# Optimization experiments

Hardware: AMD Instinct MI355X
Metric: run time of the kernel (lower is better)

## Reference

```python
import jax, jax.numpy as jnp
import numpy as np

B, S, DMODEL = 1, 2048, 4096
H, HKV, DH = 32, 8, 128
LTAB, RBKT = 20, 128
NEG = -1e9


def rotate_half(x):
    x1, x2 = x[..., : x.shape[-1] // 2], x[..., x.shape[-1] // 2:]
    return jnp.concatenate((-x2, x1), axis=-1)


def setup_inputs() -> dict:
    key = jax.random.key(0)
    ks = jax.random.split(key, 12)
    inp = {
        "hidden_states": jax.random.normal(ks[0], (B, S, DMODEL), jnp.float32),
        "cos": jax.random.uniform(ks[1], (B, S, DH), jnp.float32),
        "sin": jax.random.uniform(ks[2], (B, S, DH), jnp.float32),
        "q_probs": jax.random.uniform(ks[3], (B, H, LTAB, RBKT), jnp.float32),
        "v_norm": jax.random.uniform(ks[4], (B, H, S), jnp.float32),
        "allowed": jnp.ones((B, H, S), dtype=bool),
        "k_hard": jax.random.randint(ks[5], (B, H, LTAB, S), 0, RBKT, jnp.int32),
        "Wq": jax.random.normal(ks[6], (DMODEL, H * DH), jnp.float32) * 0.02,
        "Wk": jax.random.normal(ks[7], (DMODEL, HKV * DH), jnp.float32) * 0.02,
        "Wv": jax.random.normal(ks[8], (DMODEL, HKV * DH), jnp.float32) * 0.02,
        "Wo": jax.random.normal(ks[9], (H * DH, DMODEL), jnp.float32) * 0.02,
        "sink": 4,
        "window": 128,
        "M": 256,
    }
    return inp


def _sparse_key_mask(q_probs, v_norm, allowed, k_hard, sink, window, M):
    """Faithful jax version of build_sparse_list_decode, returned as a boolean
    allowed-key mask [B, H, T] (equivalent to scattering sparse_list)."""
    Bm, Hm, _, T = k_hard.shape
    # soft-hash collision score: sum over tables of q bucket prob at key's bucket,
    # weighted by value-norm history, restricted to allowed keys.
    coll = jnp.take_along_axis(q_probs, k_hard.astype(jnp.int32), axis=-1).sum(axis=2)  # [B,H,T]
    scores = jnp.where(allowed, coll * v_norm, -jnp.inf)
    M_eff = min(M, T)
    mask = jnp.zeros((Bm, Hm, T), dtype=bool)
    if M_eff > 0:
        heavy_idx = jax.lax.top_k(scores, M_eff)[1]  # [B,H,M]
        b_ix = jnp.arange(Bm)[:, None, None]
        h_ix = jnp.arange(Hm)[None, :, None]
        mask = mask.at[b_ix, h_ix, heavy_idx].set(True)
    sink = max(0, min(sink, T))
    window = max(0, min(window, T))
    if sink > 0:
        mask = mask.at[:, :, :sink].set(True)
    if window > 0:
        win_start = max(T - window, sink)
        if win_start < T:
            mask = mask.at[:, :, win_start:].set(True)
    if sink == 0 and window == 0:
        mask = mask.at[:, :, T - 1].set(True)
    return mask & allowed


def reference(hidden_states, cos, sin, q_probs, v_norm, allowed, k_hard,
              Wq, Wk, Wv, Wo, sink, window, M):
    Bx, Sx, _ = hidden_states.shape
    scaling = DH ** -0.5
    q = (hidden_states @ Wq).reshape(Bx, Sx, H, DH).transpose(0, 2, 1, 3)   # [B,H,S,Dh]
    k = (hidden_states @ Wk).reshape(Bx, Sx, HKV, DH).transpose(0, 2, 1, 3)  # [B,Hkv,S,Dh]
    v = (hidden_states @ Wv).reshape(Bx, Sx, HKV, DH).transpose(0, 2, 1, 3)
    # RoPE (unsqueeze_dim=1)
    c, s = cos[:, None, :, :], sin[:, None, :, :]
    q = q * c + rotate_half(q) * s
    k = k * c + rotate_half(k) * s
    # repeat_kv for GQA
    n_rep = H // HKV
    k = jnp.repeat(k, n_rep, axis=1)
    v = jnp.repeat(v, n_rep, axis=1)
    # sparse heavy-hitter + sink + window key mask (no_grad in the original)
    key_mask = _sparse_key_mask(q_probs, v_norm, allowed, k_hard, sink, window, M)  # [B,H,S]
    causal = jnp.tril(jnp.ones((Sx, Sx), dtype=bool))
    allow = causal[None, None] & key_mask[:, :, None, :]  # [B,H,S,S]
    scores = jnp.einsum('bhqd,bhkd->bhqk', q, k) * scaling
    attn = jax.nn.softmax(jnp.where(allow, scores, NEG), axis=-1)
    out = jnp.einsum('bhqk,bhkd->bhqd', attn, v)
    out = out.transpose(0, 2, 1, 3).reshape(Bx, Sx, H * DH)
    return out @ Wo
```

## Files before the change

kernel.cpp:

```cpp
#include <hip/hip_runtime.h>
#include <hip/hip_bf16.h>
#include <cstdint>
#include <cstddef>

namespace {

constexpr int S_LEN = 2048;
constexpr int DM    = 4096;
constexpr int NH    = 32;
constexpr int NKV   = 8;
constexpr int DH    = 128;
constexpr int LTAB  = 20;
constexpr int RBKT  = 128;
constexpr int NQKV  = NH * DH + 2 * NKV * DH;
constexpr int KOFF  = NH * DH;
constexpr int VOFF  = NH * DH + NKV * DH;

typedef short s16x8 __attribute__((ext_vector_type(8)));
typedef float f32x4 __attribute__((ext_vector_type(4)));
typedef unsigned long long u64;
struct u64x2 { u64 x, y; };

__device__ inline short bf16s(float f) {
  __hip_bfloat16 b = __float2bfloat16(f);
  return (short)*reinterpret_cast<unsigned short*>(&b);
}
__device__ inline float s2f(short s) {
  unsigned short u = (unsigned short)s;
  return __bfloat162float(*reinterpret_cast<__hip_bfloat16*>(&u));
}

__global__ __launch_bounds__(256) void cvt_f32_bf16(const float* __restrict__ in,
                                                    __hip_bfloat16* __restrict__ out,
                                                    int n4) {
  int i = blockIdx.x * blockDim.x + threadIdx.x;
  if (i >= n4) return;
  float4 v = reinterpret_cast<const float4*>(in)[i];
  ushort4 o;
  o.x = (unsigned short)bf16s(v.x);
  o.y = (unsigned short)bf16s(v.y);
  o.z = (unsigned short)bf16s(v.z);
  o.w = (unsigned short)bf16s(v.w);
  reinterpret_cast<ushort4*>(out)[i] = o;
}

__global__ __launch_bounds__(256) void transpose_cvt64(const float* __restrict__ W,
                                                       __hip_bfloat16* __restrict__ Wt,
                                                       int K, int N) {
  __shared__ float tile[64][65];
  const int kb = blockIdx.y * 64, nb = blockIdx.x * 64;
  const int tid = threadIdx.x;
  const int r0 = tid >> 4, c4 = (tid & 15) * 4;
#pragma unroll
  for (int it = 0; it < 4; ++it) {
    const int r = r0 + it * 16;
    float4 v = *reinterpret_cast<const float4*>(&W[(size_t)(kb + r) * N + nb + c4]);
    tile[r][c4] = v.x;
    tile[r][c4 + 1] = v.y;
    tile[r][c4 + 2] = v.z;
    tile[r][c4 + 3] = v.w;
  }
  __syncthreads();
  const int n0 = tid >> 4, k4 = (tid & 15) * 4;
#pragma unroll
  for (int it = 0; it < 4; ++it) {
    const int n = n0 + it * 16;
    ushort4 o;
    o.x = (unsigned short)bf16s(tile[k4][n]);
    o.y = (unsigned short)bf16s(tile[k4 + 1][n]);
    o.z = (unsigned short)bf16s(tile[k4 + 2][n]);
    o.w = (unsigned short)bf16s(tile[k4 + 3][n]);
    *reinterpret_cast<ushort4*>(&Wt[(size_t)(nb + n) * K + kb + k4]) = o;
  }
}

template <bool OUT_F32>
__global__ __launch_bounds__(256) void gemm_bt(const __hip_bfloat16* __restrict__ A,
                                               const __hip_bfloat16* __restrict__ Bt,
                                               void* __restrict__ Cout,
                                               int N, int K) {
  __shared__ __hip_bfloat16 As[128 * 64];
  __shared__ __hip_bfloat16 Bs[128 * 64];
  const int tid = threadIdx.x;
  const int wid = tid >> 6;
  const int lane = tid & 63;
  const int bm = blockIdx.y, bn = blockIdx.x;
  const int wr = wid >> 1, wc = wid & 1;
  f32x4 acc[4][4] = {};
  const __hip_bfloat16* Abase = A + (size_t)bm * 128 * K;
  const __hip_bfloat16* Bbase = Bt + (size_t)bn * 128 * K;
  for (int kt = 0; kt < K; kt += 64) {
    __syncthreads();
#pragma unroll
    for (int j = 0; j < 4; ++j) {
      const int pb = j * 4096 + wid * 1024;
      const int p = pb + lane * 16;
      const int row = p >> 7;
      const int slot = ((p >> 4) & 7) ^ (row & 7);
      const int goff = row * K + kt + slot * 8;
      __builtin_amdgcn_global_load_lds(
          (const __attribute__((address_space(1))) void*)(Abase + goff),
          (__attribute__((address_space(3))) void*)(As + (pb >> 1)), 16, 0, 0);
      __builtin_amdgcn_global_load_lds(
          (const __attribute__((address_space(1))) void*)(Bbase + goff),
          (__attribute__((address_space(3))) void*)(Bs + (pb >> 1)), 16, 0, 0);
    }
    __syncthreads();
#pragma unroll
    for (int kk = 0; kk < 2; ++kk) {
      s16x8 af[4], bf[4];
#pragma unroll
      for (int i = 0; i < 4; ++i) {
        const int ra = wr * 64 + i * 16 + (lane & 15);
        const int sa = (kk * 4 + (lane >> 4)) ^ (ra & 7);
        af[i] = *reinterpret_cast<const s16x8*>(As + ra * 64 + sa * 8);
        const int rb = wc * 64 + i * 16 + (lane & 15);
        const int sb = (kk * 4 + (lane >> 4)) ^ (rb & 7);
        bf[i] = *reinterpret_cast<const s16x8*>(Bs + rb * 64 + sb * 8);
      }
#pragma unroll
      for (int i = 0; i < 4; ++i)
#pragma unroll
        for (int jn = 0; jn < 4; ++jn)
          acc[i][jn] = __builtin_amdgcn_mfma_f32_16x16x32_bf16(af[i], bf[jn], acc[i][jn], 0, 0, 0);
    }
  }
  const int rg = (lane >> 4) * 4;
  const int cg = lane & 15;
#pragma unroll
  for (int i = 0; i < 4; ++i)
#pragma unroll
    for (int jn = 0; jn < 4; ++jn)
#pragma unroll
      for (int r = 0; r < 4; ++r) {
        const int rr = bm * 128 + wr * 64 + i * 16 + rg + r;
        const int cc = bn * 128 + wc * 64 + jn * 16 + cg;
        if (OUT_F32)
          reinterpret_cast<float*>(Cout)[(size_t)rr * N + cc] = acc[i][jn][r];
        else
          reinterpret_cast<__hip_bfloat16*>(Cout)[(size_t)rr * N + cc] =
              __float2bfloat16(acc[i][jn][r]);
      }
}

__global__ __launch_bounds__(256) void rope_kernel(const __hip_bfloat16* __restrict__ QKV,
                                                   const float* __restrict__ cosb,
                                                   const float* __restrict__ sinb,
                                                   __hip_bfloat16* __restrict__ Qro,
                                                   __hip_bfloat16* __restrict__ Kro) {
  const int s = blockIdx.x;
  const int tid = threadIdx.x;
  const float* cs = cosb + s * DH;
  const float* sn = sinb + s * DH;
  const __hip_bfloat16* row = QKV + (size_t)s * NQKV;
  for (int ch = tid; ch < 512 + 128; ch += 256) {
    const bool isQ = ch < 512;
    const int idx8 = (isQ ? ch : ch - 512) * 8;
    const int d8 = idx8 & (DH - 1);
    const int hb = idx8 - d8;
    const __hip_bfloat16* src = isQ ? row : row + KOFF;
    s16x8 v = *reinterpret_cast<const s16x8*>(src + idx8);
    s16x8 p = *reinterpret_cast<const s16x8*>(src + hb + (d8 ^ 64));
    const float sgn = (d8 < 64) ? -1.f : 1.f;
    s16x8 outv;
#pragma unroll
    for (int j = 0; j < 8; ++j) {
      const float r = s2f(v[j]) * cs[d8 + j] + sgn * s2f(p[j]) * sn[d8 + j];
      outv[j] = bf16s(r);
    }
    if (isQ)
      *reinterpret_cast<s16x8*>(Qro + (size_t)s * (NH * DH) + idx8) = outv;
    else
      *reinterpret_cast<s16x8*>(Kro + (size_t)s * (NKV * DH) + idx8) = outv;
  }
}

__global__ __launch_bounds__(1024) void select_kernel(const float* __restrict__ q_probs,
                                                      const float* __restrict__ v_norm,
                                                      const int* __restrict__ allowed,
                                                      const int* __restrict__ k_hard,
                                                      const int* __restrict__ sinkp,
                                                      const int* __restrict__ winp,
                                                      const int* __restrict__ Mp,
                                                      int* __restrict__ sel_idx,
                                                      int* __restrict__ sel_cnt) {
  const int h = blockIdx.x;
  const int tid = threadIdx.x;
  const int lane = tid & 63;
  const int wid = tid >> 6;
  __shared__ u64 keys[S_LEN];
  __shared__ int waveTot[16];
  const int t0 = tid * 2;
  float c0 = 0.f, c1 = 0.f;
#pragma unroll
  for (int l = 0; l < LTAB; ++l) {
    const int2 kh = *reinterpret_cast<const int2*>(&k_hard[(size_t)(h * LTAB + l) * S_LEN + t0]);
    c0 += q_probs[(h * LTAB + l) * RBKT + kh.x];
    c1 += q_probs[(h * LTAB + l) * RBKT + kh.y];
  }
  const int2 al = *reinterpret_cast<const int2*>(&allowed[h * S_LEN + t0]);
  const float2 vn = *reinterpret_cast<const float2*>(&v_norm[h * S_LEN + t0]);
  const float s0 = al.x ? c0 * vn.x : -INFINITY;
  const float s1 = al.y ? c1 * vn.y : -INFINITY;
  auto mkkey = [](float s, int t) -> u64 {
    unsigned m = __float_as_uint(s);
    m = (m & 0x80000000u) ? ~m : (m | 0x80000000u);
    return ((u64)m << 11) | (u64)(S_LEN - 1 - t);
  };
  const u64 k0 = mkkey(s0, t0);
  const u64 k1 = mkkey(s1, t0 + 1);
  keys[t0] = k0;
  keys[t0 + 1] = k1;
  __syncthreads();
  int r0 = 0, r1 = 0;
#pragma unroll 8
  for (int u = 0; u < S_LEN; u += 2) {
    const u64x2 kv = *reinterpret_cast<const u64x2*>(&keys[u]);
    r0 += (kv.x > k0) + (kv.y > k0);
    r1 += (kv.x > k1) + (kv.y > k1);
  }
  const int Mv = min(Mp[0], S_LEN);
  int sv = sinkp[0];
  sv = sv < 0 ? 0 : (sv > S_LEN ? S_LEN : sv);
  int wv = winp[0];
  wv = wv < 0 ? 0 : (wv > S_LEN ? S_LEN : wv);
  int wstart = S_LEN - wv;
  if (wstart < sv) wstart = sv;
  bool sel0 = r0 < Mv, sel1 = r1 < Mv;
  if (t0 < sv) sel0 = true;
  if (t0 + 1 < sv) sel1 = true;
  if (wv > 0) {
    if (t0 >= wstart) sel0 = true;
    if (t0 + 1 >= wstart) sel1 = true;
  }
  if (sv == 0 && wv == 0) {
    if (t0 == S_LEN - 1) sel0 = true;
    if (t0 + 1 == S_LEN - 1) sel1 = true;
  }
  sel0 = sel0 && (al.x != 0);
  sel1 = sel1 && (al.y != 0);
  const int cnt = (sel0 ? 1 : 0) + (sel1 ? 1 : 0);
  int inc = cnt;
#pragma unroll
  for (int off = 1; off < 64; off <<= 1) {
    int n = __shfl_up(inc, off);
    if (lane >= off) inc += n;
  }
  if (lane == 63) waveTot[wid] = inc;
  __syncthreads();
  int wbase = 0;
  for (int w = 0; w < wid; ++w) wbase += waveTot[w];
  int pos = wbase + inc - cnt;
  if (tid == 0) {
    int tot = 0;
#pragma unroll
    for (int w = 0; w < 16; ++w) tot += waveTot[w];
    sel_cnt[h] = tot;
  }
  if (sel0) sel_idx[h * S_LEN + pos++] = t0;
  if (sel1) sel_idx[h * S_LEN + pos] = t0 + 1;
}

__global__ __launch_bounds__(256) void attn_kernel(const __hip_bfloat16* __restrict__ Qro,
                                                   const __hip_bfloat16* __restrict__ Kro,
                                                   const __hip_bfloat16* __restrict__ Vpk,
                                                   const int* __restrict__ sel_idx,
                                                   const int* __restrict__ sel_cnt,
                                                   __hip_bfloat16* __restrict__ ctx) {
  constexpr int BKV = 32;
  const int h = blockIdx.y;
  const int q0 = blockIdx.x * 64;
  const int tid = threadIdx.x, wid = tid >> 6, lane = tid & 63;
  const int kv = h >> 2;
  __shared__ __hip_bfloat16 Ks[BKV][DH + 8];
  __shared__ __hip_bfloat16 Vt[DH][BKV + 8];
  __shared__ __hip_bfloat16 Ps[4][16][BKV + 8];
  __shared__ int tIdx[BKV];
  const int qbase = q0 + wid * 16;
  const float scaling = 0.08838834764831845f;
  s16x8 qf[4];
  {
    const __hip_bfloat16* qp =
        Qro + (size_t)(qbase + (lane & 15)) * (NH * DH) + h * DH + (lane >> 4) * 8;
#pragma unroll
    for (int kt = 0; kt < 4; ++kt) {
      s16x8 q = *reinterpret_cast<const s16x8*>(qp + kt * 32);
#pragma unroll
      for (int j = 0; j < 8; ++j) q[j] = bf16s(s2f(q[j]) * scaling);
      qf[kt] = q;
    }
  }
  s16x8 ones;
#pragma unroll
  for (int j = 0; j < 8; ++j) ones[j] = (short)0x3F80;
  float mr[4], lr[4];
#pragma unroll
  for (int r = 0; r < 4; ++r) {
    mr[r] = -3.0e38f;
    lr[r] = 0.f;
  }
  f32x4 o[8] = {};
  const int cnt = sel_cnt[h];
  const int qmax = q0 + 63;
  for (int j0 = 0; j0 < cnt; j0 += BKV) {
    if (sel_idx[h * S_LEN + j0] > qmax) break;
    const int nk = min(BKV, cnt - j0);
    __syncthreads();
    if (tid < BKV) tIdx[tid] = (tid < nk) ? sel_idx[h * S_LEN + j0 + tid] : 0x7fffffff;
#pragma unroll
    for (int c = 0; c < 2; ++c) {
      const int ch = tid + c * 256;
      const int row = ch >> 4, c8 = ch & 15;
      if (row < nk) {
        const int t = sel_idx[h * S_LEN + j0 + row];
        *reinterpret_cast<s16x8*>(&Ks[row][c8 * 8]) = *reinterpret_cast<const s16x8*>(
            Kro + (size_t)t * (NKV * DH) + kv * DH + c8 * 8);
      }
    }
    {
      const int j = tid >> 3;
      const int dp = (tid & 7) * 16;
      const int cc = j ^ (((dp >> 4) & 3) << 3);
      if (j < nk) {
        const int t = sel_idx[h * S_LEN + j0 + j];
        const __hip_bfloat16* vp = Vpk + (size_t)t * NQKV + kv * DH + dp;
        s16x8 a = *reinterpret_cast<const s16x8*>(vp);
        s16x8 b = *reinterpret_cast<const s16x8*>(vp + 8);
#pragma unroll
        for (int i = 0; i < 8; ++i) reinterpret_cast<short&>(Vt[dp + i][cc]) = a[i];
#pragma unroll
        for (int i = 0; i < 8; ++i) reinterpret_cast<short&>(Vt[dp + 8 + i][cc]) = b[i];
      } else {
#pragma unroll
        for (int i = 0; i < 16; ++i) reinterpret_cast<short&>(Vt[dp + i][cc]) = 0;
      }
    }
    __syncthreads();
    f32x4 s0 = {0.f, 0.f, 0.f, 0.f}, s1 = {0.f, 0.f, 0.f, 0.f};
#pragma unroll
    for (int kt = 0; kt < 4; ++kt) {
      s16x8 k0 = *reinterpret_cast<const s16x8*>(&Ks[lane & 15][kt * 32 + (lane >> 4) * 8]);
      s16x8 k1 = *reinterpret_cast<const s16x8*>(&Ks[16 + (lane & 15)][kt * 32 + (lane >> 4) * 8]);
      s0 = __builtin_amdgcn_mfma_f32_16x16x32_bf16(qf[kt], k0, s0, 0, 0, 0);
      s1 = __builtin_amdgcn_mfma_f32_16x16x32_bf16(qf[kt], k1, s1, 0, 0, 0);
    }
    const int t0 = tIdx[lane & 15];
    const int t1 = tIdx[16 + (lane & 15)];
    float v0[4], v1[4];
    bool need = false;
#pragma unroll
    for (int r = 0; r < 4; ++r) {
      const int qs = qbase + ((lane >> 4) << 2) + r;
      v0[r] = (t0 <= qs) ? s0[r] : -1.0e9f;
      v1[r] = (t1 <= qs) ? s1[r] : -1.0e9f;
      need = need || (fmaxf(v0[r], v1[r]) > mr[r] + 8.f);
    }
    if (__any(need)) {
#pragma unroll
      for (int r = 0; r < 4; ++r) {
        float m = fmaxf(v0[r], v1[r]);
#pragma unroll
        for (int off = 1; off < 16; off <<= 1) m = fmaxf(m, __shfl_xor(m, off));
        const float mn = fmaxf(mr[r], m);
        const float scl = __expf(mr[r] - mn);
        lr[r] *= scl;
#pragma unroll
        for (int nt = 0; nt < 8; ++nt) o[nt][r] *= scl;
        mr[r] = mn;
      }
    }
#pragma unroll
    for (int r = 0; r < 4; ++r) {
      const float p0 = __expf(v0[r] - mr[r]);
      const float p1 = __expf(v1[r] - mr[r]);
      Ps[wid][((lane >> 4) << 2) + r][lane & 15] = __float2bfloat16(p0);
      Ps[wid][((lane >> 4) << 2) + r][16 + (lane & 15)] = __float2bfloat16(p1);
    }
    const s16x8 pf = *reinterpret_cast<const s16x8*>(&Ps[wid][lane & 15][(lane >> 4) * 8]);
    {
      f32x4 zero = {0.f, 0.f, 0.f, 0.f};
      f32x4 psum = __builtin_amdgcn_mfma_f32_16x16x32_bf16(pf, ones, zero, 0, 0, 0);
#pragma unroll
      for (int r = 0; r < 4; ++r) lr[r] += psum[r];
    }
#pragma unroll
    for (int nt = 0; nt < 8; ++nt) {
      const s16x8 vf = *reinterpret_cast<const s16x8*>(
          &Vt[nt * 16 + (lane & 15)][(((lane >> 4) ^ nt) & 3) * 8]);
      o[nt] = __builtin_amdgcn_mfma_f32_16x16x32_bf16(pf, vf, o[nt], 0, 0, 0);
    }
  }
#pragma unroll
  for (int nt = 0; nt < 8; ++nt)
#pragma unroll
    for (int r = 0; r < 4; ++r) {
      const int qs = qbase + ((lane >> 4) << 2) + r;
      const int d = nt * 16 + (lane & 15);
      ctx[(size_t)qs * (NH * DH) + h * DH + d] = __float2bfloat16(o[nt][r] / lr[r]);
    }
}

}

extern "C" void kernel_launch(void* const* d_in, const int* in_sizes, int n_in,
                              void* d_out, int out_size, void* d_ws, size_t ws_size,
                              hipStream_t stream) {
  const float* hidden = (const float*)d_in[0];
  const float* cosb = (const float*)d_in[1];
  const float* sinb = (const float*)d_in[2];
  const float* q_probs = (const float*)d_in[3];
  const float* v_norm = (const float*)d_in[4];
  const int* allowed = (const int*)d_in[5];
  const int* k_hard = (const int*)d_in[6];
  const float* Wq = (const float*)d_in[7];
  const float* Wk = (const float*)d_in[8];
  const float* Wv = (const float*)d_in[9];
  const float* Wo = (const float*)d_in[10];
  const int* sinkp = (const int*)d_in[11];
  const int* winp = (const int*)d_in[12];
  const int* Mp = (const int*)d_in[13];

  char* ws = (char*)d_ws;
  size_t off = 0;
  auto alloc = [&](size_t bytes) -> char* {
    char* p = ws + off;
    off += (bytes + 255) & ~(size_t)255;
    return p;
  };
  __hip_bfloat16* hbf = (__hip_bfloat16*)alloc((size_t)S_LEN * DM * 2);
  __hip_bfloat16* WqkvT = (__hip_bfloat16*)alloc((size_t)NQKV * DM * 2);
  __hip_bfloat16* WoT = (__hip_bfloat16*)alloc((size_t)DM * DM * 2);
  __hip_bfloat16* QKV = (__hip_bfloat16*)alloc((size_t)S_LEN * NQKV * 2);
  __hip_bfloat16* Qro = (__hip_bfloat16*)alloc((size_t)S_LEN * NH * DH * 2);
  __hip_bfloat16* Kro = (__hip_bfloat16*)alloc((size_t)S_LEN * NKV * DH * 2);
  __hip_bfloat16* ctx = (__hip_bfloat16*)alloc((size_t)S_LEN * NH * DH * 2);
  int* sel_idx = (int*)alloc((size_t)NH * S_LEN * 4);
  int* sel_cnt = (int*)alloc((size_t)NH * 4);
  if (off > ws_size) return;

  {
    const int n4 = S_LEN * DM / 4;
    cvt_f32_bf16<<<(n4 + 255) / 256, 256, 0, stream>>>(hidden, hbf, n4);
  }
  transpose_cvt64<<<dim3(DM / 64, DM / 64), 256, 0, stream>>>(Wq, WqkvT, DM, DM);
  transpose_cvt64<<<dim3((NKV * DH) / 64, DM / 64), 256, 0, stream>>>(
      Wk, WqkvT + (size_t)KOFF * DM, DM, NKV * DH);
  transpose_cvt64<<<dim3((NKV * DH) / 64, DM / 64), 256, 0, stream>>>(
      Wv, WqkvT + (size_t)VOFF * DM, DM, NKV * DH);
  transpose_cvt64<<<dim3(DM / 64, DM / 64), 256, 0, stream>>>(Wo, WoT, DM, DM);

  gemm_bt<false><<<dim3(NQKV / 128, S_LEN / 128), 256, 0, stream>>>(
      hbf, WqkvT, (void*)QKV, NQKV, DM);

  rope_kernel<<<S_LEN, 256, 0, stream>>>(QKV, cosb, sinb, Qro, Kro);

  select_kernel<<<NH, 1024, 0, stream>>>(q_probs, v_norm, allowed, k_hard, sinkp, winp, Mp,
                                         sel_idx, sel_cnt);

  attn_kernel<<<dim3(S_LEN / 64, NH), 256, 0, stream>>>(Qro, Kro, QKV + VOFF, sel_idx,
                                                        sel_cnt, ctx);

  gemm_bt<true><<<dim3(DM / 128, S_LEN / 128), 256, 0, stream>>>(ctx, WoT, d_out, DM, DM);
}
```

Baseline: 411.9 us.

## Fuse prep conversion kernels and enlarge attention key tile to 64

Merges the hidden-state conversion and four weight transpose-convert launches into a single prep kernel to cut launch overhead. In the attention kernel, the key/value tile grows from 32 to 64 keys, with a wider XOR swizzle for the transposed V buffer and twice the MFMAs per tile. This halves loop iterations and barriers over the sparse key list, but increases shared memory and may process more masked keys near the causal boundary.

```diff
diff --git a/kernel.cpp b/kernel.cpp
--- a/kernel.cpp
+++ b/kernel.cpp
@@ -30,26 +30,46 @@
   return __bfloat162float(*reinterpret_cast<__hip_bfloat16*>(&u));
 }
 
-__global__ __launch_bounds__(256) void cvt_f32_bf16(const float* __restrict__ in,
-                                                    __hip_bfloat16* __restrict__ out,
-                                                    int n4) {
-  int i = blockIdx.x * blockDim.x + threadIdx.x;
-  if (i >= n4) return;
-  float4 v = reinterpret_cast<const float4*>(in)[i];
-  ushort4 o;
-  o.x = (unsigned short)bf16s(v.x);
-  o.y = (unsigned short)bf16s(v.y);
-  o.z = (unsigned short)bf16s(v.z);
-  o.w = (unsigned short)bf16s(v.w);
-  reinterpret_cast<ushort4*>(out)[i] = o;
-}
-
-__global__ __launch_bounds__(256) void transpose_cvt64(const float* __restrict__ W,
-                                                       __hip_bfloat16* __restrict__ Wt,
-                                                       int K, int N) {
+__global__ __launch_bounds__(256) void prep_kernel(const float* __restrict__ hidden,
+                                                   const float* __restrict__ Wq,
+                                                   const float* __restrict__ Wk,
+                                                   const float* __restrict__ Wv,
+                                                   const float* __restrict__ Wo,
+                                                   __hip_bfloat16* __restrict__ hbf,
+                                                   __hip_bfloat16* __restrict__ WqkvT,
+                                                   __hip_bfloat16* __restrict__ WoT) {
   __shared__ float tile[64][65];
-  const int kb = blockIdx.y * 64, nb = blockIdx.x * 64;
-  const int tid = threadIdx.x;
+  const int b = blockIdx.x, tid = threadIdx.x;
+  if (b < 2048) {
+    const size_t base = (size_t)b * 1024;
+#pragma unroll
+    for (int it = 0; it < 4; ++it) {
+      const size_t i = base + it * 256 + tid;
+      float4 v = reinterpret_cast<const float4*>(hidden)[i];
+      ushort4 o;
+      o.x = (unsigned short)bf16s(v.x);
+      o.y = (unsigned short)bf16s(v.y);
+      o.z = (unsigned short)bf16s(v.z);
+      o.w = (unsigned short)bf16s(v.w);
+      reinterpret_cast<ushort4*>(hbf)[i] = o;
+    }
+    return;
+  }
+  const float* W;
+  __hip_bfloat16* Wt;
+  int N, bx, by;
+  int t = b - 2048;
+  if (t < 4096) {
+    W = Wq; Wt = WqkvT; N = DM; bx = t & 63; by = t >> 6;
+  } else if (t < 5120) {
+    t -= 4096; W = Wk; Wt = WqkvT + (size_t)KOFF * DM; N = NKV * DH; bx = t & 15; by = t >> 4;
+  } else if (t < 6144) {
+    t -= 5120; W = Wv; Wt = WqkvT + (size_t)VOFF * DM; N = NKV * DH; bx = t & 15; by = t >> 4;
+  } else {
+    t -= 6144; W = Wo; Wt = WoT; N = DM; bx = t & 63; by = t >> 6;
+  }
+  const int K = DM;
+  const int kb = by * 64, nb = bx * 64;
   const int r0 = tid >> 4, c4 = (tid & 15) * 4;
 #pragma unroll
   for (int it = 0; it < 4; ++it) {
@@ -267,10 +287,11 @@
                                                    const int* __restrict__ sel_idx,
                                                    const int* __restrict__ sel_cnt,
                                                    __hip_bfloat16* __restrict__ ctx) {
-  constexpr int BKV = 32;
+  constexpr int BKV = 64;
   const int h = blockIdx.y;
   const int q0 = blockIdx.x * 64;
   const int tid = threadIdx.x, wid = tid >> 6, lane = tid & 63;
+  const int l15 = lane & 15, hi = lane >> 4;
   const int kv = h >> 2;
   __shared__ __hip_bfloat16 Ks[BKV][DH + 8];
   __shared__ __hip_bfloat16 Vt[DH][BKV + 8];
@@ -281,7 +302,7 @@
   s16x8 qf[4];
   {
     const __hip_bfloat16* qp =
-        Qro + (size_t)(qbase + (lane & 15)) * (NH * DH) + h * DH + (lane >> 4) * 8;
+        Qro + (size_t)(qbase + l15) * (NH * DH) + h * DH + hi * 8;
 #pragma unroll
     for (int kt = 0; kt < 4; ++kt) {
       s16x8 q = *reinterpret_cast<const s16x8*>(qp + kt * 32);
@@ -308,7 +329,7 @@
     __syncthreads();
     if (tid < BKV) tIdx[tid] = (tid < nk) ? sel_idx[h * S_LEN + j0 + tid] : 0x7fffffff;
 #pragma unroll
-    for (int c = 0; c < 2; ++c) {
+    for (int c = 0; c < 4; ++c) {
       const int ch = tid + c * 256;
       const int row = ch >> 4, c8 = ch & 15;
       if (row < nk) {
@@ -318,47 +339,65 @@
       }
     }
     {
-      const int j = tid >> 3;
-      const int dp = (tid & 7) * 16;
-      const int cc = j ^ (((dp >> 4) & 3) << 3);
+      const int j = tid >> 2;
+      const int dp = (tid & 3) * 32;
+      const int ccA = j ^ (((dp >> 4) & 7) << 3);
+      const int ccB = j ^ ((((dp >> 4) + 1) & 7) << 3);
       if (j < nk) {
         const int t = sel_idx[h * S_LEN + j0 + j];
         const __hip_bfloat16* vp = Vpk + (size_t)t * NQKV + kv * DH + dp;
         s16x8 a = *reinterpret_cast<const s16x8*>(vp);
-        s16x8 b = *reinterpret_cast<const s16x8*>(vp + 8);
-#pragma unroll
-        for (int i = 0; i < 8; ++i) reinterpret_cast<short&>(Vt[dp + i][cc]) = a[i];
-#pragma unroll
-        for (int i = 0; i < 8; ++i) reinterpret_cast<short&>(Vt[dp + 8 + i][cc]) = b[i];
+        s16x8 bq = *reinterpret_cast<const s16x8*>(vp + 8);
+        s16x8 cq = *reinterpret_cast<const s16x8*>(vp + 16);
+        s16x8 dq = *reinterpret_cast<const s16x8*>(vp + 24);
+#pragma unroll
+        for (int i = 0; i < 8; ++i) reinterpret_cast<short&>(Vt[dp + i][ccA]) = a[i];
+#pragma unroll
+        for (int i = 0; i < 8; ++i) reinterpret_cast<short&>(Vt[dp + 8 + i][ccA]) = bq[i];
+#pragma unroll
+        for (int i = 0; i < 8; ++i) reinterpret_cast<short&>(Vt[dp + 16 + i][ccB]) = cq[i];
+#pragma unroll
+        for (int i = 0; i < 8; ++i) reinterpret_cast<short&>(Vt[dp + 24 + i][ccB]) = dq[i];
       } else {
 #pragma unroll
-        for (int i = 0; i < 16; ++i) reinterpret_cast<short&>(Vt[dp + i][cc]) = 0;
+        for (int i = 0; i < 16; ++i) reinterpret_cast<short&>(Vt[dp + i][ccA]) = 0;
+#pragma unroll
+        for (int i = 0; i < 16; ++i) reinterpret_cast<short&>(Vt[dp + 16 + i][ccB]) = 0;
       }
     }
     __syncthreads();
-    f32x4 s0 = {0.f, 0.f, 0.f, 0.f}, s1 = {0.f, 0.f, 0.f, 0.f};
+    f32x4 sc[4];
+#pragma unroll
+    for (int kc = 0; kc < 4; ++kc) sc[kc] = f32x4{0.f, 0.f, 0.f, 0.f};
 #pragma unroll
     for (int kt = 0; kt < 4; ++kt) {
-      s16x8 k0 = *reinterpret_cast<const s16x8*>(&Ks[lane & 15][kt * 32 + (lane >> 4) * 8]);
-      s16x8 k1 = *reinterpret_cast<const s16x8*>(&Ks[16 + (lane & 15)][kt * 32 + (lane >> 4) * 8]);
-      s0 = __builtin_amdgcn_mfma_f32_16x16x32_bf16(qf[kt], k0, s0, 0, 0, 0);
-      s1 = __builtin_amdgcn_mfma_f32_16x16x32_bf16(qf[kt], k1, s1, 0, 0, 0);
-    }
-    const int t0 = tIdx[lane & 15];
-    const int t1 = tIdx[16 + (lane & 15)];
-    float v0[4], v1[4];
+#pragma unroll
+      for (int kc = 0; kc < 4; ++kc) {
+        const s16x8 kf =
+            *reinterpret_cast<const s16x8*>(&Ks[kc * 16 + l15][kt * 32 + hi * 8]);
+        sc[kc] = __builtin_amdgcn_mfma_f32_16x16x32_bf16(qf[kt], kf, sc[kc], 0, 0, 0);
+      }
+    }
+    int tt[4];
+#pragma unroll
+    for (int kc = 0; kc < 4; ++kc) tt[kc] = tIdx[kc * 16 + l15];
+    float vv[4][4];
     bool need = false;
 #pragma unroll
     for (int r = 0; r < 4; ++r) {
-      const int qs = qbase + ((lane >> 4) << 2) + r;
-      v0[r] = (t0 <= qs) ? s0[r] : -1.0e9f;
-      v1[r] = (t1 <= qs) ? s1[r] : -1.0e9f;
-      need = need || (fmaxf(v0[r], v1[r]) > mr[r] + 8.f);
+      const int qs = qbase + (hi << 2) + r;
+      float mx = -3.0e38f;
+#pragma unroll
+      for (int kc = 0; kc < 4; ++kc) {
+        vv[kc][r] = (tt[kc] <= qs) ? sc[kc][r] : -1.0e9f;
+        mx = fmaxf(mx, vv[kc][r]);
+      }
+      need = need || (mx > mr[r] + 8.f);
     }
     if (__any(need)) {
 #pragma unroll
       for (int r = 0; r < 4; ++r) {
-        float m = fmaxf(v0[r], v1[r]);
+        float m = fmaxf(fmaxf(vv[0][r], vv[1][r]), fmaxf(vv[2][r], vv[3][r]));
 #pragma unroll
         for (int off = 1; off < 16; off <<= 1) m = fmaxf(m, __shfl_xor(m, off));
         const float mn = fmaxf(mr[r], m);
@@ -371,31 +410,36 @@
     }
 #pragma unroll
     for (int r = 0; r < 4; ++r) {
-      const float p0 = __expf(v0[r] - mr[r]);
-      const float p1 = __expf(v1[r] - mr[r]);
-      Ps[wid][((lane >> 4) << 2) + r][lane & 15] = __float2bfloat16(p0);
-      Ps[wid][((lane >> 4) << 2) + r][16 + (lane & 15)] = __float2bfloat16(p1);
-    }
-    const s16x8 pf = *reinterpret_cast<const s16x8*>(&Ps[wid][lane & 15][(lane >> 4) * 8]);
+#pragma unroll
+      for (int kc = 0; kc < 4; ++kc) {
+        Ps[wid][(hi << 2) + r][kc * 16 + l15] = __float2bfloat16(__expf(vv[kc][r] - mr[r]));
+      }
+    }
+    const s16x8 pf0 = *reinterpret_cast<const s16x8*>(&Ps[wid][l15][hi * 8]);
+    const s16x8 pf1 = *reinterpret_cast<const s16x8*>(&Ps[wid][l15][32 + hi * 8]);
     {
       f32x4 zero = {0.f, 0.f, 0.f, 0.f};
-      f32x4 psum = __builtin_amdgcn_mfma_f32_16x16x32_bf16(pf, ones, zero, 0, 0, 0);
-#pragma unroll
-      for (int r = 0; r < 4; ++r) lr[r] += psum[r];
+      f32x4 ps = __builtin_amdgcn_mfma_f32_16x16x32_bf16(pf0, ones, zero, 0, 0, 0);
+      ps = __builtin_amdgcn_mfma_f32_16x16x32_bf16(pf1, ones, ps, 0, 0, 0);
+#pragma unroll
+      for (int r = 0; r < 4; ++r) lr[r] += ps[r];
     }
 #pragma unroll
     for (int nt = 0; nt < 8; ++nt) {
-      const s16x8 vf = *reinterpret_cast<const s16x8*>(
-          &Vt[nt * 16 + (lane & 15)][(((lane >> 4) ^ nt) & 3) * 8]);
-      o[nt] = __builtin_amdgcn_mfma_f32_16x16x32_bf16(pf, vf, o[nt], 0, 0, 0);
+      const s16x8 vfa =
+          *reinterpret_cast<const s16x8*>(&Vt[nt * 16 + l15][(hi * 8) ^ (nt * 8)]);
+      const s16x8 vfb =
+          *reinterpret_cast<const s16x8*>(&Vt[nt * 16 + l15][(32 + hi * 8) ^ (nt * 8)]);
+      o[nt] = __builtin_amdgcn_mfma_f32_16x16x32_bf16(pf0, vfa, o[nt], 0, 0, 0);
+      o[nt] = __builtin_amdgcn_mfma_f32_16x16x32_bf16(pf1, vfb, o[nt], 0, 0, 0);
     }
   }
 #pragma unroll
   for (int nt = 0; nt < 8; ++nt)
 #pragma unroll
     for (int r = 0; r < 4; ++r) {
-      const int qs = qbase + ((lane >> 4) << 2) + r;
-      const int d = nt * 16 + (lane & 15);
+      const int qs = qbase + (hi << 2) + r;
+      const int d = nt * 16 + l15;
       ctx[(size_t)qs * (NH * DH) + h * DH + d] = __float2bfloat16(o[nt][r] / lr[r]);
     }
 }
@@ -438,16 +482,7 @@
   int* sel_cnt = (int*)alloc((size_t)NH * 4);
   if (off > ws_size) return;
 
-  {
-    const int n4 = S_LEN * DM / 4;
-    cvt_f32_bf16<<<(n4 + 255) / 256, 256, 0, stream>>>(hidden, hbf, n4);
-  }
-  transpose_cvt64<<<dim3(DM / 64, DM / 64), 256, 0, stream>>>(Wq, WqkvT, DM, DM);
-  transpose_cvt64<<<dim3((NKV * DH) / 64, DM / 64), 256, 0, stream>>>(
-      Wk, WqkvT + (size_t)KOFF * DM, DM, NKV * DH);
-  transpose_cvt64<<<dim3((NKV * DH) / 64, DM / 64), 256, 0, stream>>>(
-      Wv, WqkvT + (size_t)VOFF * DM, DM, NKV * DH);
-  transpose_cvt64<<<dim3(DM / 64, DM / 64), 256, 0, stream>>>(Wo, WoT, DM, DM);
+  prep_kernel<<<12288, 256, 0, stream>>>(hidden, Wq, Wk, Wv, Wo, hbf, WqkvT, WoT);
 
   gemm_bt<false><<<dim3(NQKV / 128, S_LEN / 128), 256, 0, stream>>>(
       hbf, WqkvT, (void*)QKV, NQKV, DM);
```

Result: faster. 387.7 us (-5.9%).
